# Optimization experiments

Measured on AMD Instinct MI355X. Metric: run time of the kernel, lower is better.

## Reference

```python
import jax, jax.numpy as jnp
import numpy as np

B, S, D = 2, 1024, 2048
H, HKV, HD = 16, 4, 128


def _rotate_half(x):
    x1, x2 = jnp.split(x, 2, axis=-1)
    return jnp.concatenate([-x2, x1], axis=-1)


def setup_inputs() -> dict:
    key = jax.random.key(0)
    ks = jax.random.split(key, 8)
    hidden_states = jax.random.normal(ks[0], (B, S, D), dtype=jnp.float32)
    position_ids = jnp.tile(jnp.arange(S, dtype=jnp.int32)[None, :], (B, 1))
    active_mask = jax.random.bernoulli(ks[1], 0.5, (B, S))
    active_mask = active_mask.at[:, 0].set(True)  # ensure >=1 causal valid key per query
    # standard RoPE tables
    inv_freq = 1.0 / (10000.0 ** (jnp.arange(0, HD, 2, dtype=jnp.float32) / HD))
    freqs = jnp.arange(S, dtype=jnp.float32)[:, None] * inv_freq[None, :]
    emb = jnp.concatenate([freqs, freqs], axis=-1)  # [S, HD]
    cos, sin = jnp.cos(emb), jnp.sin(emb)
    scale = 0.02
    wq = jax.random.normal(ks[2], (D, H * HD), dtype=jnp.float32) * scale
    wk = jax.random.normal(ks[3], (D, HKV * HD), dtype=jnp.float32) * scale
    wv = jax.random.normal(ks[4], (D, HKV * HD), dtype=jnp.float32) * scale
    wo = jax.random.normal(ks[5], (H * HD, D), dtype=jnp.float32) * scale
    return {"hidden_states": hidden_states, "cos": cos, "sin": sin,
            "wq": wq, "wk": wk, "wv": wv, "wo": wo,
            "position_ids": position_ids, "active_mask": active_mask}


def reference(hidden_states, cos, sin, wq, wk, wv, wo, position_ids, active_mask):
    b, s, d = hidden_states.shape
    groups = H // HKV
    scale = HD ** -0.5

    q = (hidden_states @ wq).reshape(b, s, H, HD).transpose(0, 2, 1, 3)    # [b,H,s,hd]
    k = (hidden_states @ wk).reshape(b, s, HKV, HD).transpose(0, 2, 1, 3)  # [b,Hkv,s,hd]
    v = (hidden_states @ wv).reshape(b, s, HKV, HD).transpose(0, 2, 1, 3)

    cs, sn = cos[None, None], sin[None, None]  # [1,1,s,hd]
    q = q * cs + _rotate_half(q) * sn
    k = k * cs + _rotate_half(k) * sn

    # SelectiveKVCache.update_selective (prefill from empty cache):
    # per-batch gather of active tokens, padded (k/v with 0, positions with -1).
    # Padding to full s is math-equivalent to padding to max_active (padded
    # slots are masked with -inf below).
    ar = jnp.arange(s, dtype=jnp.int32)
    order = jnp.argsort(jnp.where(active_mask, ar, ar + s), axis=1)        # actives first, stable order
    sorted_mask = jnp.take_along_axis(active_mask, order, axis=1)          # [b,s]
    gidx = order[:, None, :, None]
    k_sel = jnp.take_along_axis(k, gidx, axis=2) * sorted_mask[:, None, :, None]
    v_sel = jnp.take_along_axis(v, gidx, axis=2) * sorted_mask[:, None, :, None]
    pos_sel = jnp.where(sorted_mask, jnp.take_along_axis(position_ids, order, axis=1), -1)  # [b,s]

    # GQA: repeat kv heads
    k_rep = jnp.repeat(k_sel, groups, axis=1)  # [b,H,skv,hd]
    v_rep = jnp.repeat(v_sel, groups, axis=1)

    scores = jnp.einsum('bhqd,bhkd->bhqk', q, k_rep) * scale
    valid = (pos_sel >= 0)[:, None, None, :]                               # [b,1,1,skv]
    causal = (pos_sel[:, None, :] <= position_ids[:, :, None])[:, None]    # [b,1,q,skv]
    big_neg = jnp.finfo(scores.dtype).min
    scores = jnp.where(valid & causal, scores, big_neg)

    attn = jax.nn.softmax(scores, axis=-1)
    out = jnp.einsum('bhqk,bhkd->bhqd', attn, v_rep)
    out = out.transpose(0, 2, 1, 3).reshape(b, s, H * HD)
    return out @ wo
```

## Files before the change

kernel.cpp:

```cpp
#include <hip/hip_runtime.h>
#include <hip/hip_bf16.h>

#define Bn 2
#define Sn 1024
#define Dn 2048
#define Hn 16
#define HKVn 4
#define HDn 128

typedef __attribute__((ext_vector_type(8))) short s8v;
typedef __attribute__((ext_vector_type(8))) unsigned short u8v;
typedef __attribute__((ext_vector_type(4))) float f4v;
typedef __hip_bfloat16 bf16;

typedef __attribute__((address_space(3))) void lds_void;
typedef __attribute__((address_space(1))) const void gbl_void;
#define ASYNC_LD16(g, l) \
  __builtin_amdgcn_global_load_lds((gbl_void*)(g), (lds_void*)(l), 16, 0, 0)

static __device__ __forceinline__ unsigned short f2b_bits(float f) {
  bf16 h = __float2bfloat16(f);
  return __builtin_bit_cast(unsigned short, h);
}

__global__ void mask_norm(const void* __restrict__ mraw, unsigned char* __restrict__ m8, int n) {
  __shared__ int bytemode;
  if (threadIdx.x == 0) bytemode = 0;
  __syncthreads();
  const unsigned int* mi = (const unsigned int*)mraw;
  int local = 0;
  for (int t = threadIdx.x; t < n / 4; t += blockDim.x)
    if (mi[t] > 1u) local = 1;
  if (local) atomicOr(&bytemode, 1);
  __syncthreads();
  const int bm = bytemode;
  const unsigned char* mb = (const unsigned char*)mraw;
  for (int t = threadIdx.x; t < n; t += blockDim.x)
    m8[t] = bm ? (mb[t] ? 1 : 0) : (mi[t] != 0u ? 1 : 0);
}

__global__ void cvt_bf16(const float* __restrict__ src, bf16* __restrict__ dst, int n8) {
  int stride = gridDim.x * blockDim.x;
  for (int i = blockIdx.x * blockDim.x + threadIdx.x; i < n8; i += stride) {
    float4 a = reinterpret_cast<const float4*>(src)[2 * i];
    float4 b = reinterpret_cast<const float4*>(src)[2 * i + 1];
    u8v o;
    o[0] = f2b_bits(a.x); o[1] = f2b_bits(a.y); o[2] = f2b_bits(a.z); o[3] = f2b_bits(a.w);
    o[4] = f2b_bits(b.x); o[5] = f2b_bits(b.y); o[6] = f2b_bits(b.z); o[7] = f2b_bits(b.w);
    reinterpret_cast<u8v*>(dst)[i] = o;
  }
}

__global__ __launch_bounds__(256) void transpose_all(
    const float* __restrict__ s0, const float* __restrict__ s1,
    const float* __restrict__ s2, const float* __restrict__ s3,
    bf16* __restrict__ d0, bf16* __restrict__ d1, bf16* __restrict__ d2, bf16* __restrict__ d3) {
  __shared__ float tile[64][65];
  const int z = blockIdx.z;
  const float* src = (z == 0) ? s0 : (z == 1) ? s1 : (z == 2) ? s2 : s3;
  bf16* dst = (z == 0) ? d0 : (z == 1) ? d1 : (z == 2) ? d2 : d3;
  const int N = (z == 1 || z == 2) ? 512 : 2048;
  const int K = Dn;
  const int bx = blockIdx.x * 64;
  if (bx >= N) return;
  const int by = blockIdx.y * 64;
  const int t = threadIdx.x;
  const int lr = t >> 4, lc4 = (t & 15) * 4;
  #pragma unroll
  for (int it = 0; it < 4; ++it) {
    int k = it * 16 + lr;
    float4 v = *reinterpret_cast<const float4*>(&src[(size_t)(by + k) * N + bx + lc4]);
    tile[k][lc4] = v.x; tile[k][lc4 + 1] = v.y; tile[k][lc4 + 2] = v.z; tile[k][lc4 + 3] = v.w;
  }
  __syncthreads();
  #pragma unroll
  for (int it = 0; it < 4; ++it) {
    int n = it * 16 + lr;
    ushort4 o;
    o.x = f2b_bits(tile[lc4 + 0][n]);
    o.y = f2b_bits(tile[lc4 + 1][n]);
    o.z = f2b_bits(tile[lc4 + 2][n]);
    o.w = f2b_bits(tile[lc4 + 3][n]);
    *reinterpret_cast<ushort4*>(&dst[(size_t)(bx + n) * K + by + lc4]) = o;
  }
}

template <int EPI>
__global__ __launch_bounds__(256) void gemm_nt(
    const bf16* __restrict__ A, const bf16* __restrict__ Bt,
    bf16* __restrict__ Oq, bf16* __restrict__ Ok, bf16* __restrict__ Ov,
    float* __restrict__ Of, int K, int N, int nbx) {
  __shared__ __align__(16) bf16 Al[2][128 * 64];
  __shared__ __align__(16) bf16 Bl[2][128 * 64];
  const int tid = threadIdx.x;
  const int lane = tid & 63, w = tid >> 6;
  const int wm = (w >> 1) * 64, wn = (w & 1) * 64;
  const int nwg = gridDim.x;
  const int flat = blockIdx.x;
  const int swz = (flat & 7) * (nwg >> 3) + (flat >> 3);
  const int m0 = (swz / nbx) * 128, n0 = (swz % nbx) * 128;
  const int l16 = lane & 15, lg = lane >> 4;
  const int srow = lane >> 3;
  const int sch = lane & 7;
  f4v acc[4][4] = {};
  const int nt = K >> 6;

  auto stage = [&](int buf, int k0) {
    #pragma unroll
    for (int i = 0; i < 4; ++i) {
      const int rb = w * 32 + i * 8;
      const int r = rb + srow;
      const int cs = (sch ^ (r & 7)) * 8;
      ASYNC_LD16(&A[(size_t)(m0 + r) * K + k0 + cs], &Al[buf][rb * 64]);
      ASYNC_LD16(&Bt[(size_t)(n0 + r) * K + k0 + cs], &Bl[buf][rb * 64]);
    }
  };

  stage(0, 0);
  __syncthreads();

  for (int t = 0; t < nt; ++t) {
    const int cur = t & 1;
    if (t + 1 < nt) stage(cur ^ 1, (t + 1) << 6);
    #pragma unroll
    for (int kc = 0; kc < 2; ++kc) {
      s8v af[4], bfr[4];
      #pragma unroll
      for (int mf = 0; mf < 4; ++mf) {
        int r = wm + mf * 16 + l16;
        af[mf] = *reinterpret_cast<const s8v*>(&Al[cur][r * 64 + (((kc * 4 + lg) ^ (r & 7)) * 8)]);
      }
      #pragma unroll
      for (int nf = 0; nf < 4; ++nf) {
        int r = wn + nf * 16 + l16;
        bfr[nf] = *reinterpret_cast<const s8v*>(&Bl[cur][r * 64 + (((kc * 4 + lg) ^ (r & 7)) * 8)]);
      }
      #pragma unroll
      for (int mf = 0; mf < 4; ++mf)
        #pragma unroll
        for (int nf = 0; nf < 4; ++nf)
          acc[mf][nf] = __builtin_amdgcn_mfma_f32_16x16x32_bf16(af[mf], bfr[nf], acc[mf][nf], 0, 0, 0);
    }
    __syncthreads();
  }
  #pragma unroll
  for (int mf = 0; mf < 4; ++mf) {
    #pragma unroll
    for (int nf = 0; nf < 4; ++nf) {
      #pragma unroll
      for (int i = 0; i < 4; ++i) {
        int gm = m0 + wm + mf * 16 + lg * 4 + i;
        int gn = n0 + wn + nf * 16 + l16;
        float v = acc[mf][nf][i];
        if (EPI == 0) {
          int b = gm >> 10, s = gm & 1023;
          if (gn < 2048) {
            int h = gn >> 7, hd = gn & 127;
            Oq[(((size_t)(b * Hn + h)) * Sn + s) * HDn + hd] = __float2bfloat16(v);
          } else if (gn < 2560) {
            int t2 = gn - 2048, kvh = t2 >> 7, hd = t2 & 127;
            Ok[(((size_t)(b * HKVn + kvh)) * Sn + s) * HDn + hd] = __float2bfloat16(v);
          } else {
            int t2 = gn - 2560, kvh = t2 >> 7, hd = t2 & 127;
            Ov[(((size_t)(b * HKVn + kvh)) * HDn + hd) * Sn + s] = __float2bfloat16(v);
          }
        } else {
          Of[(size_t)gm * N + gn] = v;
        }
      }
    }
  }
}

__global__ void rope_qk(bf16* __restrict__ qb, bf16* __restrict__ kb,
                        const float* __restrict__ cosp, const float* __restrict__ sinp) {
  const int NQ = Bn * Hn * Sn * 16;
  const int NT = NQ + Bn * HKVn * Sn * 16;
  int stride = gridDim.x * blockDim.x;
  for (int idx = blockIdx.x * blockDim.x + threadIdx.x; idx < NT; idx += stride) {
    bf16* base;
    int rel;
    if (idx < NQ) { base = qb; rel = idx; }
    else          { base = kb; rel = idx - NQ; }
    int d4 = (rel & 15) * 4;
    int s = (rel >> 4) & 1023;
    int head = rel >> 14;
    bf16* p = base + ((size_t)head * Sn + s) * HDn + d4;
    ushort4 a = *reinterpret_cast<ushort4*>(p);
    ushort4 b = *reinterpret_cast<ushort4*>(p + 64);
    float4 c = *reinterpret_cast<const float4*>(&cosp[s * HDn + d4]);
    float4 sv = *reinterpret_cast<const float4*>(&sinp[s * HDn + d4]);
    float x1[4] = {__bfloat162float(__builtin_bit_cast(bf16, a.x)), __bfloat162float(__builtin_bit_cast(bf16, a.y)),
                   __bfloat162float(__builtin_bit_cast(bf16, a.z)), __bfloat162float(__builtin_bit_cast(bf16, a.w))};
    float x2[4] = {__bfloat162float(__builtin_bit_cast(bf16, b.x)), __bfloat162float(__builtin_bit_cast(bf16, b.y)),
                   __bfloat162float(__builtin_bit_cast(bf16, b.z)), __bfloat162float(__builtin_bit_cast(bf16, b.w))};
    float cc[4] = {c.x, c.y, c.z, c.w};
    float ss[4] = {sv.x, sv.y, sv.z, sv.w};
    ushort4 o1, o2;
    unsigned short* o1p = &o1.x; unsigned short* o2p = &o2.x;
    #pragma unroll
    for (int j = 0; j < 4; ++j) {
      o1p[j] = f2b_bits(x1[j] * cc[j] - x2[j] * ss[j]);
      o2p[j] = f2b_bits(x2[j] * cc[j] + x1[j] * ss[j]);
    }
    *reinterpret_cast<ushort4*>(p) = o1;
    *reinterpret_cast<ushort4*>(p + 64) = o2;
  }
}

__global__ __launch_bounds__(256) void attn_fwd(
    const bf16* __restrict__ q, const bf16* __restrict__ k, const bf16* __restrict__ vT,
    const unsigned char* __restrict__ m8, bf16* __restrict__ out) {
  __shared__ __align__(16) bf16 Kl[2][64 * 128];
  __shared__ __align__(16) bf16 Vl[2][128 * 64];
  __shared__ __align__(16) bf16 Pl[4][16 * 72];
  const int tid = threadIdx.x;
  const int lane = tid & 63, w = tid >> 6;
  const int l16 = lane & 15, lg = lane >> 4;
  const int qx = blockIdx.x, h = blockIdx.y, b = blockIdx.z;
  const int NQT = Sn / 64;
  const int qt = (b == 1) ? (NQT - 1 - qx) : qx;
  const int hkv = h >> 2;
  const int q0 = qt * 64 + w * 16;
  const float sl2 = 0.08838834764831845f * 1.44269504088896f;

  const bf16* qp = q + ((size_t)(b * Hn + h) * Sn + q0) * HDn;
  const bf16* kp = k + (size_t)(b * HKVn + hkv) * Sn * HDn;
  const bf16* vp = vT + (size_t)(b * HKVn + hkv) * HDn * Sn;
  const unsigned char* mp = m8 + b * Sn;

  auto stage = [&](int buf, int kbase) {
    #pragma unroll
    for (int i = 0; i < 4; ++i) {
      int ci = i * 256 + w * 64 + lane;
      int kr = ci >> 4, kch = ci & 15;
      ASYNC_LD16(kp + (size_t)(kbase + kr) * HDn + ((kch ^ (kr & 7)) * 8),
                 &Kl[buf][(i * 256 + w * 64) * 8]);
      int vr = ci >> 3, vch = ci & 7;
      ASYNC_LD16(vp + (size_t)vr * Sn + kbase + ((vch ^ (vr & 7)) * 8),
                 &Vl[buf][(i * 256 + w * 64) * 8]);
    }
  };

  s8v qf[4];
  #pragma unroll
  for (int hc = 0; hc < 4; ++hc)
    qf[hc] = *reinterpret_cast<const s8v*>(qp + l16 * HDn + hc * 32 + lg * 8);

  float mrow[4], lrow[4];
  f4v o[8] = {};
  #pragma unroll
  for (int i = 0; i < 4; ++i) { mrow[i] = -1e30f; lrow[i] = 0.f; }

  stage(0, 0);
  __syncthreads();

  for (int kt = 0; kt <= qt; ++kt) {
    const int cur = kt & 1;
    const int kb = kt * 64;
    if (kt < qt) stage(cur ^ 1, kb + 64);

    f4v sc[4] = {};
    #pragma unroll
    for (int ktc = 0; ktc < 4; ++ktc) {
      #pragma unroll
      for (int hc = 0; hc < 4; ++hc) {
        int r = ktc * 16 + l16;
        s8v kf = *reinterpret_cast<const s8v*>(
            &Kl[cur][r * 128 + (((hc * 4 + lg) ^ (r & 7)) * 8)]);
        sc[ktc] = __builtin_amdgcn_mfma_f32_16x16x32_bf16(qf[hc], kf, sc[ktc], 0, 0, 0);
      }
    }
    float pm[4];
    #pragma unroll
    for (int i = 0; i < 4; ++i) pm[i] = -1e30f;
    int act[4];
    #pragma unroll
    for (int ktc = 0; ktc < 4; ++ktc) act[ktc] = mp[kb + ktc * 16 + l16];
    if (kt == qt) {
      #pragma unroll
      for (int ktc = 0; ktc < 4; ++ktc) {
        int j = kb + ktc * 16 + l16;
        #pragma unroll
        for (int i = 0; i < 4; ++i) {
          int qr = q0 + lg * 4 + i;
          float v = sc[ktc][i] * sl2;
          v = (act[ktc] && j <= qr) ? v : -1e30f;
          sc[ktc][i] = v;
          pm[i] = fmaxf(pm[i], v);
        }
      }
    } else {
      #pragma unroll
      for (int ktc = 0; ktc < 4; ++ktc) {
        #pragma unroll
        for (int i = 0; i < 4; ++i) {
          float v = sc[ktc][i] * sl2;
          v = act[ktc] ? v : -1e30f;
          sc[ktc][i] = v;
          pm[i] = fmaxf(pm[i], v);
        }
      }
    }
    #pragma unroll
    for (int off = 1; off < 16; off <<= 1)
      #pragma unroll
      for (int i = 0; i < 4; ++i) pm[i] = fmaxf(pm[i], __shfl_xor(pm[i], off, 64));
    float fac[4];
    #pragma unroll
    for (int i = 0; i < 4; ++i) {
      float mn = fmaxf(mrow[i], pm[i]);
      fac[i] = exp2f(mrow[i] - mn);
      mrow[i] = mn;
    }
    float rs[4] = {0.f, 0.f, 0.f, 0.f};
    #pragma unroll
    for (int ktc = 0; ktc < 4; ++ktc)
      #pragma unroll
      for (int i = 0; i < 4; ++i) {
        float p = exp2f(sc[ktc][i] - mrow[i]);
        rs[i] += p;
        Pl[w][(lg * 4 + i) * 72 + ktc * 16 + l16] = __float2bfloat16(p);
      }
    #pragma unroll
    for (int off = 1; off < 16; off <<= 1)
      #pragma unroll
      for (int i = 0; i < 4; ++i) rs[i] += __shfl_xor(rs[i], off, 64);
    #pragma unroll
    for (int i = 0; i < 4; ++i) lrow[i] = lrow[i] * fac[i] + rs[i];
    #pragma unroll
    for (int fn = 0; fn < 8; ++fn)
      #pragma unroll
      for (int i = 0; i < 4; ++i) o[fn][i] *= fac[i];
    #pragma unroll
    for (int kc = 0; kc < 2; ++kc) {
      s8v pf = *reinterpret_cast<const s8v*>(&Pl[w][l16 * 72 + kc * 32 + lg * 8]);
      #pragma unroll
      for (int fn = 0; fn < 8; ++fn) {
        int d = fn * 16 + l16;
        s8v vf = *reinterpret_cast<const s8v*>(
            &Vl[cur][d * 64 + (((kc * 4 + lg) ^ (d & 7)) * 8)]);
        o[fn] = __builtin_amdgcn_mfma_f32_16x16x32_bf16(pf, vf, o[fn], 0, 0, 0);
      }
    }
    __syncthreads();
  }
  #pragma unroll
  for (int fn = 0; fn < 8; ++fn)
    #pragma unroll
    for (int i = 0; i < 4; ++i) {
      int qr = q0 + lg * 4 + i;
      out[((size_t)b * Sn + qr) * (Hn * HDn) + h * HDn + fn * 16 + l16] =
          __float2bfloat16(o[fn][i] / lrow[i]);
    }
}

extern "C" void kernel_launch(void* const* d_in, const int* in_sizes, int n_in,
                              void* d_out, int out_size, void* d_ws, size_t ws_size,
                              hipStream_t stream) {
  const float* hs   = (const float*)d_in[0];
  const float* cosp = (const float*)d_in[1];
  const float* sinp = (const float*)d_in[2];
  const float* wq   = (const float*)d_in[3];
  const float* wk   = (const float*)d_in[4];
  const float* wv   = (const float*)d_in[5];
  const float* wo   = (const float*)d_in[6];
  const void*  am   = d_in[8];

  char* ws = (char*)d_ws;
  bf16* WT  = (bf16*)(ws);
  bf16* woT = (bf16*)(ws + 12582912);
  bf16* qb  = (bf16*)(ws + 12582912 + 8388608);
  bf16* kb  = (bf16*)(ws + 12582912 + 16777216);
  bf16* vT  = (bf16*)(ws + 12582912 + 18874368);
  bf16* ao  = (bf16*)(ws + 12582912 + 20971520);
  unsigned char* m8 = (unsigned char*)(ws + 12582912 + 29360128);
  bf16* hsb = (bf16*)d_out;
  float* outp = (float*)d_out;

  mask_norm<<<1, 256, 0, stream>>>(am, m8, Bn * Sn);
  cvt_bf16<<<2048, 256, 0, stream>>>(hs, hsb, (Bn * Sn * Dn) / 8);
  transpose_all<<<dim3(32, 32, 4), 256, 0, stream>>>(
      wq, wk, wv, wo, WT, WT + (size_t)2048 * Dn, WT + (size_t)2560 * Dn, woT);
  gemm_nt<0><<<384, 256, 0, stream>>>(hsb, WT, qb, kb, vT, nullptr, Dn, 3072, 24);
  rope_qk<<<1024, 256, 0, stream>>>(qb, kb, cosp, sinp);
  attn_fwd<<<dim3(Sn / 64, Hn, Bn), 256, 0, stream>>>(qb, kb, vT, m8, ao);
  gemm_nt<1><<<256, 256, 0, stream>>>(ao, woT, nullptr, nullptr, nullptr, outp, Hn * HDn, Dn, 16);
}
```

Before: 238.1 us.

## Merge prep kernels into one launch and fuse Q RoPE into attention

The mask normalization, hidden-state bf16 conversion and weight transposes now run as one launch, with block ranges assigned to each job. Q RoPE moves into the attention kernel's Q-fragment load, so a separate read-modify-write pass over the Q tensor disappears. A smaller rope_k kernel still handles K. This removes two launches and a large memory pass, at the cost of extra cos/sin loads per attention block and the rope arithmetic now running inside attention.

Result: no change. 233.6 us (-1.9%).

```diff
diff --git a/kernel.cpp b/kernel.cpp
--- a/kernel.cpp
+++ b/kernel.cpp
@@ -22,49 +22,58 @@
   bf16 h = __float2bfloat16(f);
   return __builtin_bit_cast(unsigned short, h);
 }
-
-__global__ void mask_norm(const void* __restrict__ mraw, unsigned char* __restrict__ m8, int n) {
-  __shared__ int bytemode;
-  if (threadIdx.x == 0) bytemode = 0;
-  __syncthreads();
-  const unsigned int* mi = (const unsigned int*)mraw;
-  int local = 0;
-  for (int t = threadIdx.x; t < n / 4; t += blockDim.x)
-    if (mi[t] > 1u) local = 1;
-  if (local) atomicOr(&bytemode, 1);
-  __syncthreads();
-  const int bm = bytemode;
-  const unsigned char* mb = (const unsigned char*)mraw;
-  for (int t = threadIdx.x; t < n; t += blockDim.x)
-    m8[t] = bm ? (mb[t] ? 1 : 0) : (mi[t] != 0u ? 1 : 0);
-}
-
-__global__ void cvt_bf16(const float* __restrict__ src, bf16* __restrict__ dst, int n8) {
-  int stride = gridDim.x * blockDim.x;
-  for (int i = blockIdx.x * blockDim.x + threadIdx.x; i < n8; i += stride) {
-    float4 a = reinterpret_cast<const float4*>(src)[2 * i];
-    float4 b = reinterpret_cast<const float4*>(src)[2 * i + 1];
-    u8v o;
-    o[0] = f2b_bits(a.x); o[1] = f2b_bits(a.y); o[2] = f2b_bits(a.z); o[3] = f2b_bits(a.w);
-    o[4] = f2b_bits(b.x); o[5] = f2b_bits(b.y); o[6] = f2b_bits(b.z); o[7] = f2b_bits(b.w);
-    reinterpret_cast<u8v*>(dst)[i] = o;
-  }
-}
-
-__global__ __launch_bounds__(256) void transpose_all(
-    const float* __restrict__ s0, const float* __restrict__ s1,
-    const float* __restrict__ s2, const float* __restrict__ s3,
-    bf16* __restrict__ d0, bf16* __restrict__ d1, bf16* __restrict__ d2, bf16* __restrict__ d3) {
+static __device__ __forceinline__ float b2f(short u) {
+  return __bfloat162float(__builtin_bit_cast(bf16, (unsigned short)u));
+}
+
+__global__ __launch_bounds__(256) void prep(
+    const float* __restrict__ hs, bf16* __restrict__ hsb,
+    const float* __restrict__ wq, const float* __restrict__ wk,
+    const float* __restrict__ wv, const float* __restrict__ wo,
+    bf16* __restrict__ WT, bf16* __restrict__ woT,
+    const void* __restrict__ am, unsigned char* __restrict__ m8) {
+  const int bid = blockIdx.x;
+  const int t = threadIdx.x;
+  if (bid < 1024) {
+    const int n8 = (Bn * Sn * Dn) / 8;
+    for (int i = bid * 256 + t; i < n8; i += 1024 * 256) {
+      float4 a = reinterpret_cast<const float4*>(hs)[2 * i];
+      float4 b = reinterpret_cast<const float4*>(hs)[2 * i + 1];
+      u8v o;
+      o[0] = f2b_bits(a.x); o[1] = f2b_bits(a.y); o[2] = f2b_bits(a.z); o[3] = f2b_bits(a.w);
+      o[4] = f2b_bits(b.x); o[5] = f2b_bits(b.y); o[6] = f2b_bits(b.z); o[7] = f2b_bits(b.w);
+      reinterpret_cast<u8v*>(hsb)[i] = o;
+    }
+    return;
+  }
+  if (bid == 3584) {
+    __shared__ int bytemode;
+    if (t == 0) bytemode = 0;
+    __syncthreads();
+    const int n = Bn * Sn;
+    const unsigned int* mi = (const unsigned int*)am;
+    int local = 0;
+    for (int i = t; i < n / 4; i += 256)
+      if (mi[i] > 1u) local = 1;
+    if (local) atomicOr(&bytemode, 1);
+    __syncthreads();
+    const int bm = bytemode;
+    const unsigned char* mb = (const unsigned char*)am;
+    for (int i = t; i < n; i += 256)
+      m8[i] = bm ? (mb[i] ? 1 : 0) : (mi[i] != 0u ? 1 : 0);
+    return;
+  }
   __shared__ float tile[64][65];
-  const int z = blockIdx.z;
-  const float* src = (z == 0) ? s0 : (z == 1) ? s1 : (z == 2) ? s2 : s3;
-  bf16* dst = (z == 0) ? d0 : (z == 1) ? d1 : (z == 2) ? d2 : d3;
-  const int N = (z == 1 || z == 2) ? 512 : 2048;
-  const int K = Dn;
-  const int bx = blockIdx.x * 64;
-  if (bx >= N) return;
-  const int by = blockIdx.y * 64;
-  const int t = threadIdx.x;
+  const float* src;
+  bf16* dst;
+  int N, local;
+  if (bid < 2048)      { src = wq; dst = WT;                          N = 2048; local = bid - 1024; }
+  else if (bid < 2304) { src = wk; dst = WT + (size_t)2048 * Dn;      N = 512;  local = bid - 2048; }
+  else if (bid < 2560) { src = wv; dst = WT + (size_t)2560 * Dn;      N = 512;  local = bid - 2304; }
+  else                 { src = wo; dst = woT;                         N = 2048; local = bid - 2560; }
+  const int nbx = N / 64;
+  const int bx = (local % nbx) * 64;
+  const int by = (local / nbx) * 64;
   const int lr = t >> 4, lc4 = (t & 15) * 4;
   #pragma unroll
   for (int it = 0; it < 4; ++it) {
@@ -81,7 +90,7 @@
     o.y = f2b_bits(tile[lc4 + 1][n]);
     o.z = f2b_bits(tile[lc4 + 2][n]);
     o.w = f2b_bits(tile[lc4 + 3][n]);
-    *reinterpret_cast<ushort4*>(&dst[(size_t)(bx + n) * K + by + lc4]) = o;
+    *reinterpret_cast<ushort4*>(&dst[(size_t)(bx + n) * Dn + by + lc4]) = o;
   }
 }
 
@@ -172,45 +181,38 @@
   }
 }
 
-__global__ void rope_qk(bf16* __restrict__ qb, bf16* __restrict__ kb,
-                        const float* __restrict__ cosp, const float* __restrict__ sinp) {
-  const int NQ = Bn * Hn * Sn * 16;
-  const int NT = NQ + Bn * HKVn * Sn * 16;
-  int stride = gridDim.x * blockDim.x;
-  for (int idx = blockIdx.x * blockDim.x + threadIdx.x; idx < NT; idx += stride) {
-    bf16* base;
-    int rel;
-    if (idx < NQ) { base = qb; rel = idx; }
-    else          { base = kb; rel = idx - NQ; }
-    int d4 = (rel & 15) * 4;
-    int s = (rel >> 4) & 1023;
-    int head = rel >> 14;
-    bf16* p = base + ((size_t)head * Sn + s) * HDn + d4;
-    ushort4 a = *reinterpret_cast<ushort4*>(p);
-    ushort4 b = *reinterpret_cast<ushort4*>(p + 64);
-    float4 c = *reinterpret_cast<const float4*>(&cosp[s * HDn + d4]);
-    float4 sv = *reinterpret_cast<const float4*>(&sinp[s * HDn + d4]);
-    float x1[4] = {__bfloat162float(__builtin_bit_cast(bf16, a.x)), __bfloat162float(__builtin_bit_cast(bf16, a.y)),
-                   __bfloat162float(__builtin_bit_cast(bf16, a.z)), __bfloat162float(__builtin_bit_cast(bf16, a.w))};
-    float x2[4] = {__bfloat162float(__builtin_bit_cast(bf16, b.x)), __bfloat162float(__builtin_bit_cast(bf16, b.y)),
-                   __bfloat162float(__builtin_bit_cast(bf16, b.z)), __bfloat162float(__builtin_bit_cast(bf16, b.w))};
-    float cc[4] = {c.x, c.y, c.z, c.w};
-    float ss[4] = {sv.x, sv.y, sv.z, sv.w};
-    ushort4 o1, o2;
-    unsigned short* o1p = &o1.x; unsigned short* o2p = &o2.x;
-    #pragma unroll
-    for (int j = 0; j < 4; ++j) {
-      o1p[j] = f2b_bits(x1[j] * cc[j] - x2[j] * ss[j]);
-      o2p[j] = f2b_bits(x2[j] * cc[j] + x1[j] * ss[j]);
-    }
-    *reinterpret_cast<ushort4*>(p) = o1;
-    *reinterpret_cast<ushort4*>(p + 64) = o2;
-  }
+__global__ void rope_k(bf16* __restrict__ kb,
+                       const float* __restrict__ cosp, const float* __restrict__ sinp) {
+  const int NT = Bn * HKVn * Sn * 16;
+  int idx = blockIdx.x * blockDim.x + threadIdx.x;
+  if (idx >= NT) return;
+  int d4 = (idx & 15) * 4;
+  int s = (idx >> 4) & 1023;
+  int head = idx >> 14;
+  bf16* p = kb + ((size_t)head * Sn + s) * HDn + d4;
+  ushort4 a = *reinterpret_cast<ushort4*>(p);
+  ushort4 b = *reinterpret_cast<ushort4*>(p + 64);
+  float4 c = *reinterpret_cast<const float4*>(&cosp[s * HDn + d4]);
+  float4 sv = *reinterpret_cast<const float4*>(&sinp[s * HDn + d4]);
+  float x1[4] = {b2f((short)a.x), b2f((short)a.y), b2f((short)a.z), b2f((short)a.w)};
+  float x2[4] = {b2f((short)b.x), b2f((short)b.y), b2f((short)b.z), b2f((short)b.w)};
+  float cc[4] = {c.x, c.y, c.z, c.w};
+  float ss[4] = {sv.x, sv.y, sv.z, sv.w};
+  ushort4 o1, o2;
+  unsigned short* o1p = &o1.x; unsigned short* o2p = &o2.x;
+  #pragma unroll
+  for (int j = 0; j < 4; ++j) {
+    o1p[j] = f2b_bits(x1[j] * cc[j] - x2[j] * ss[j]);
+    o2p[j] = f2b_bits(x2[j] * cc[j] + x1[j] * ss[j]);
+  }
+  *reinterpret_cast<ushort4*>(p) = o1;
+  *reinterpret_cast<ushort4*>(p + 64) = o2;
 }
 
 __global__ __launch_bounds__(256) void attn_fwd(
     const bf16* __restrict__ q, const bf16* __restrict__ k, const bf16* __restrict__ vT,
-    const unsigned char* __restrict__ m8, bf16* __restrict__ out) {
+    const unsigned char* __restrict__ m8, bf16* __restrict__ out,
+    const float* __restrict__ cosp, const float* __restrict__ sinp) {
   __shared__ __align__(16) bf16 Kl[2][64 * 128];
   __shared__ __align__(16) bf16 Vl[2][128 * 64];
   __shared__ __align__(16) bf16 Pl[4][16 * 72];
@@ -243,9 +245,32 @@
   };
 
   s8v qf[4];
-  #pragma unroll
-  for (int hc = 0; hc < 4; ++hc)
-    qf[hc] = *reinterpret_cast<const s8v*>(qp + l16 * HDn + hc * 32 + lg * 8);
+  {
+    s8v qraw[4];
+    #pragma unroll
+    for (int hc = 0; hc < 4; ++hc)
+      qraw[hc] = *reinterpret_cast<const s8v*>(qp + l16 * HDn + hc * 32 + lg * 8);
+    const float* cb = cosp + (size_t)(q0 + l16) * HDn;
+    const float* sb = sinp + (size_t)(q0 + l16) * HDn;
+    #pragma unroll
+    for (int hc = 0; hc < 2; ++hc) {
+      #pragma unroll
+      for (int jj = 0; jj < 2; ++jj) {
+        float4 c4 = *reinterpret_cast<const float4*>(cb + hc * 32 + lg * 8 + jj * 4);
+        float4 s4 = *reinterpret_cast<const float4*>(sb + hc * 32 + lg * 8 + jj * 4);
+        float cc[4] = {c4.x, c4.y, c4.z, c4.w};
+        float ss[4] = {s4.x, s4.y, s4.z, s4.w};
+        #pragma unroll
+        for (int j = 0; j < 4; ++j) {
+          int e = jj * 4 + j;
+          float lo = b2f(qraw[hc][e]);
+          float hi = b2f(qraw[hc + 2][e]);
+          qf[hc][e]     = (short)f2b_bits(lo * cc[j] - hi * ss[j]);
+          qf[hc + 2][e] = (short)f2b_bits(hi * cc[j] + lo * ss[j]);
+        }
+      }
+    }
+  }
 
   float mrow[4], lrow[4];
   f4v o[8] = {};
@@ -378,12 +403,9 @@
   bf16* hsb = (bf16*)d_out;
   float* outp = (float*)d_out;
 
-  mask_norm<<<1, 256, 0, stream>>>(am, m8, Bn * Sn);
-  cvt_bf16<<<2048, 256, 0, stream>>>(hs, hsb, (Bn * Sn * Dn) / 8);
-  transpose_all<<<dim3(32, 32, 4), 256, 0, stream>>>(
-      wq, wk, wv, wo, WT, WT + (size_t)2048 * Dn, WT + (size_t)2560 * Dn, woT);
+  prep<<<3585, 256, 0, stream>>>(hs, hsb, wq, wk, wv, wo, WT, woT, am, m8);
   gemm_nt<0><<<384, 256, 0, stream>>>(hsb, WT, qb, kb, vT, nullptr, Dn, 3072, 24);
-  rope_qk<<<1024, 256, 0, stream>>>(qb, kb, cosp, sinp);
-  attn_fwd<<<dim3(Sn / 64, Hn, Bn), 256, 0, stream>>>(qb, kb, vT, m8, ao);
+  rope_k<<<512, 256, 0, stream>>>(kb, cosp, sinp);
+  attn_fwd<<<dim3(Sn / 64, Hn, Bn), 256, 0, stream>>>(qb, kb, vT, m8, ao, cosp, sinp);
   gemm_nt<1><<<256, 256, 0, stream>>>(ao, woT, nullptr, nullptr, nullptr, outp, Hn * HDn, Dn, 16);
 }
```
